# Kernel optimization log

Measured on AMD Instinct MI355X. Metric: run time of the kernel, lower is better.

## Reference

```python
import jax, jax.numpy as jnp
import numpy as np

D_MODEL = 1024
NUM_SLOTS = 64
TOP_K = 8
B, T = 4, 4096


def setup_inputs() -> dict:
    key = jax.random.key(0)
    ks = jax.random.split(key, 16)
    D, S = D_MODEL, NUM_SLOTS
    H = D // 2  # route MLP hidden (hardcoded d_model//2 in source)
    sc = lambda fan_in: 1.0 / np.sqrt(fan_in)
    inp = {
        "x": jax.random.normal(ks[0], (B, T, D), dtype=jnp.float32),
        # learned params
        "slot_init": jax.random.normal(ks[1], (S, D), dtype=jnp.float32) * 0.1,
        "slot_scale": jnp.ones((S, 1), dtype=jnp.float32),
        "w1": jax.random.normal(ks[2], (H, 2 * D), dtype=jnp.float32) * sc(2 * D),
        "b1": jnp.zeros((H,), dtype=jnp.float32),
        "w2": jax.random.normal(ks[3], (S, H), dtype=jnp.float32) * sc(H),
        "b2": jnp.zeros((S,), dtype=jnp.float32),
        "gru_wih": jax.random.normal(ks[4], (3 * D, D), dtype=jnp.float32) * sc(D),
        "gru_whh": jax.random.normal(ks[5], (3 * D, D), dtype=jnp.float32) * sc(D),
        "gru_bih": jnp.zeros((3 * D,), dtype=jnp.float32),
        "gru_bhh": jnp.zeros((3 * D,), dtype=jnp.float32),
        "wv": jax.random.normal(ks[6], (D, D), dtype=jnp.float32) * sc(D),
        "bv": jnp.zeros((D,), dtype=jnp.float32),
        "wo": jax.random.normal(ks[7], (D, D), dtype=jnp.float32) * sc(D),
        "bo": jnp.zeros((D,), dtype=jnp.float32),
        "tau": jnp.ones((1,), dtype=jnp.float32),
    }
    return inp


def _forward(x, slot_init, slot_scale, w1, b1, w2, b2,
             gru_wih, gru_whh, gru_bih, gru_bhh, wv, bv, wo, bo, tau):
    Bn, Tn, D = x.shape
    Sn = slot_init.shape[0]
    # initial slot states, expanded over batch: (B, S, D)
    S = jnp.broadcast_to((slot_init * slot_scale)[None], (Bn, Sn, D)).astype(x.dtype)
    slot_mean = S.mean(axis=1, keepdims=True)                      # (B,1,D)
    ctx = jnp.concatenate([x, jnp.broadcast_to(slot_mean, x.shape)], axis=-1)  # (B,T,2D)
    h = jax.nn.gelu(ctx @ w1.T + b1, approximate=False)
    route_logits = (h @ w2.T + b2) / (jnp.abs(tau) + 0.1)          # (B,T,S)
    topk_vals, topk_idx = jax.lax.top_k(route_logits, TOP_K)
    topk_w = jax.nn.softmax(topk_vals, axis=-1)                    # (B,T,K)
    # scatter top-k weights into dense alpha (B,T,S)
    alpha = jnp.sum(topk_w[..., None] * jax.nn.one_hot(topk_idx, Sn, dtype=x.dtype), axis=-2)
    slot_input = jnp.einsum('bts,btd->bsd', alpha, x)              # dispatch
    slot_wsum = alpha.sum(axis=1) + 1e-8                           # (B,S)
    gi = (slot_input / slot_wsum[..., None]).reshape(Bn * Sn, D)
    hs = S.reshape(Bn * Sn, D)
    # GRUCell (torch semantics)
    gx = gi @ gru_wih.T + gru_bih                                  # (BS, 3D)
    gh = hs @ gru_whh.T + gru_bhh
    xr, xz, xn = jnp.split(gx, 3, axis=-1)
    hr, hz, hn = jnp.split(gh, 3, axis=-1)
    r = jax.nn.sigmoid(xr + hr)
    z = jax.nn.sigmoid(xz + hz)
    n = jnp.tanh(xn + r * hn)
    h_new = (1.0 - z) * n + z * hs
    S_new = h_new.reshape(Bn, Sn, D)
    slot_values = S_new @ wv.T + bv                                # (B,S,D)
    out = jnp.einsum('bts,bsd->btd', alpha, slot_values)           # combine
    return out @ wo.T + bo


def reference(x, slot_init, slot_scale, w1, b1, w2, b2,
              gru_wih, gru_whh, gru_bih, gru_bhh, wv, bv, wo, bo, tau):
    return _forward(x, slot_init, slot_scale, w1, b1, w2, b2,
                    gru_wih, gru_whh, gru_bih, gru_bhh, wv, bv, wo, bo, tau)
```

## Files before the change

### kernel.cpp

```cpp
#include <hip/hip_runtime.h>

using u16 = unsigned short;
using u32 = unsigned int;

typedef __attribute__((ext_vector_type(8))) short bf16x8;
typedef __attribute__((ext_vector_type(4))) float f32x4;

#define NTOK 16384

constexpr size_t OFF_FLAG   = 0;
constexpr size_t OFF_FCNT   = 256;
constexpr size_t OFF_M      = 512;
constexpr size_t OFF_B1P64  = 8704;
constexpr size_t OFF_B1P32  = 12800;
constexpr size_t OFF_B2F    = 14848;
constexpr size_t OFF_BIHF   = 15104;
constexpr size_t OFF_BHHF   = 27392;
constexpr size_t OFF_BVF    = 39680;
constexpr size_t OFF_BOF    = 43776;
constexpr size_t OFF_FLAGS  = 47872;
constexpr size_t OFF_HSHI   = 113408;
constexpr size_t OFF_HSLO   = 244480;
constexpr size_t OFF_HSF    = 375552;
constexpr size_t OFF_GH     = 637696;
constexpr size_t OFF_GIHI   = 1424128;
constexpr size_t OFF_GILO   = 1948416;
constexpr size_t OFF_GX     = 2472704;
constexpr size_t OFF_SNHI   = 5618432;
constexpr size_t OFF_SNLO   = 6142720;
constexpr size_t OFF_SVHI   = 6667008;
constexpr size_t OFF_SVLO   = 7191296;
constexpr size_t OFF_SVO    = 7715584;
constexpr size_t OFF_IDX    = 8764160;
constexpr size_t OFF_WGT    = 9288448;
constexpr size_t OFF_LOGITS = 9812736;
constexpr size_t OFF_W1HI   = 14007040;
constexpr size_t OFF_W1LO   = 16104192;
constexpr size_t OFF_W2HI   = 18201344;
constexpr size_t OFF_W2LO   = 18266880;
constexpr size_t OFF_WIHHI  = 18332416;
constexpr size_t OFF_WIHLO  = 24623872;
constexpr size_t OFF_WHHHI  = 30915328;
constexpr size_t OFF_WHHLO  = 37206784;
constexpr size_t OFF_WVHI   = 43498240;
constexpr size_t OFF_WVLO   = 45595392;
constexpr size_t OFF_WOHI   = 47692544;
constexpr size_t OFF_WOLO   = 49789696;
constexpr size_t OFF_HHI    = 51886848;
constexpr size_t OFF_HLO    = 68664064;
constexpr size_t OFF_DPART  = 85441280;
constexpr size_t OFF_DWSUM  = 93829888;
constexpr size_t OFF_HSMG   = 93838080;
constexpr size_t WS_NEED    = 94886656;

constexpr int QCAP = 256;

__device__ __forceinline__ float bf2f(u16 u) {
  union { u32 i; float f; } c; c.i = ((u32)u) << 16; return c.f;
}
__device__ __forceinline__ u16 f2bf(float f) {
  u32 x = __float_as_uint(f);
  x += 0x7fffu + ((x >> 16) & 1u);
  return (u16)(x >> 16);
}
__device__ __forceinline__ void splitf(float v, u16& hi, u16& lo) {
  hi = f2bf(v);
  lo = f2bf(v - bf2f(hi));
}
__device__ __forceinline__ float rdval(const void* p, int i, int f32m) {
  return f32m ? ((const float*)p)[i] : bf2f(((const u16*)p)[i]);
}
__device__ __forceinline__ void async16(const u16* g, u16* l) {
  __builtin_amdgcn_global_load_lds((const __attribute__((address_space(1))) void*)g,
                                   (__attribute__((address_space(3))) void*)l, 16, 0, 0);
}

__global__ void k_sniff(const u32* __restrict__ w1w, int* __restrict__ flag) {
  int t = threadIdx.x;
  u32 word = w1w[t * 97];
  int ef = (word >> 7) & 0xFF;
  unsigned long long m = __ballot(ef >= 128);
  if (t == 0) flag[0] = (__popcll(m) >= 8) ? 1 : 0;
}

__global__ __launch_bounds__(256) void k_cvt_all(
    const void* __restrict__ w1, const void* __restrict__ w2,
    const void* __restrict__ wih, const void* __restrict__ whh,
    const void* __restrict__ wv, const void* __restrict__ wo,
    const void* __restrict__ b2, const void* __restrict__ bih,
    const void* __restrict__ bhh, const void* __restrict__ bv,
    const void* __restrict__ bo, char* __restrict__ ws,
    const int* __restrict__ flagp)
{
  const int f = *flagp;
  const long long gid = (long long)blockIdx.x * 256 + threadIdx.x;
  const long long C0 = 1048576, C1 = C0 + 32768, C2 = C1 + 3145728,
                  C3 = C2 + 3145728, C4 = C3 + 1048576, C5 = C4 + 1048576;
  if (gid < C5) {
    const void* src; size_t oh, ol; int i;
    if (gid < C0)      { src = w1;  oh = OFF_W1HI;  ol = OFF_W1LO;  i = (int)gid; }
    else if (gid < C1) { src = w2;  oh = OFF_W2HI;  ol = OFF_W2LO;  i = (int)(gid - C0); }
    else if (gid < C2) { src = wih; oh = OFF_WIHHI; ol = OFF_WIHLO; i = (int)(gid - C1); }
    else if (gid < C3) { src = whh; oh = OFF_WHHHI; ol = OFF_WHHLO; i = (int)(gid - C2); }
    else if (gid < C4) { src = wv;  oh = OFF_WVHI;  ol = OFF_WVLO;  i = (int)(gid - C3); }
    else               { src = wo;  oh = OFF_WOHI;  ol = OFF_WOLO;  i = (int)(gid - C4); }
    float v = rdval(src, i, f);
    u16 hi, lo; splitf(v, hi, lo);
    ((u16*)(ws + oh))[i] = hi;
    ((u16*)(ws + ol))[i] = lo;
    return;
  }
  int r = (int)(gid - C5);
  if (r >= 8256) return;
  const void* src; size_t od; int i;
  if (r < 64)        { src = b2;  od = OFF_B2F;  i = r; }
  else if (r < 3136) { src = bih; od = OFF_BIHF; i = r - 64; }
  else if (r < 6208) { src = bhh; od = OFF_BHHF; i = r - 3136; }
  else if (r < 7232) { src = bv;  od = OFF_BVF;  i = r - 6208; }
  else               { src = bo;  od = OFF_BOF;  i = r - 7232; }
  ((float*)(ws + od))[i] = rdval(src, i, f);
}

template<int MODE>
__global__ __launch_bounds__(512, 2) void gemm_bt(
    const u16* __restrict__ Ahi, const u16* __restrict__ Alo,
    const u16* __restrict__ Bhi, const u16* __restrict__ Blo,
    int M, int N, int K, int ldb,
    const float* __restrict__ biasF, float* __restrict__ outF,
    u16* __restrict__ outHi, u16* __restrict__ outLo)
{
  __shared__ alignas(16) u16 smem[2 * 2 * 8192];
  const int t    = threadIdx.x;
  const int grp  = t >> 8;
  const int tl   = t & 255;
  const int wvid = tl >> 6;
  const int lane = t & 63;
  const int quad = lane >> 4;
  const int l16  = lane & 15;
  const int row0 = blockIdx.x * 128;
  const int col0 = blockIdx.y * 128;
  const int wr   = (wvid >> 1) * 64;
  const int wc   = (wvid & 1) * 64;

  const int ra  = tl >> 2;
  const int kqe = (tl & 3) * 8;
  int r_a0 = row0 + ra;      if (r_a0 > M - 1) r_a0 = M - 1;
  int r_a1 = row0 + ra + 64; if (r_a1 > M - 1) r_a1 = M - 1;
  int r_b0 = col0 + ra;      if (r_b0 > N - 1) r_b0 = N - 1;
  int r_b1 = col0 + ra + 64; if (r_b1 > N - 1) r_b1 = N - 1;
  const size_t aoff0 = (size_t)r_a0 * K + kqe;
  const size_t aoff1 = (size_t)r_a1 * K + kqe;
  const size_t boff0 = (size_t)r_b0 * ldb + kqe;
  const size_t boff1 = (size_t)r_b1 * ldb + kqe;

  const int KH  = K >> 1;
  const int NIT = 3 * (KH >> 5);
  int sp = 0, sk = grp * KH;
  const int skend = grp * KH + KH;

  u16* const base = smem + grp * 16384;
  auto stage = [&](int buf) {
    const u16* Ap = (sp == 1) ? Alo : Ahi;
    const u16* Bp = (sp == 2) ? Blo : Bhi;
    u16* At = base + buf * 8192;
    u16* Bt = At + 4096;
    async16(Ap + aoff0 + sk, &At[(wvid * 64) * 8]);
    async16(Ap + aoff1 + sk, &At[(wvid * 64 + 256) * 8]);
    async16(Bp + boff0 + sk, &Bt[(wvid * 64) * 8]);
    async16(Bp + boff1 + sk, &Bt[(wvid * 64 + 256) * 8]);
    sk += 32;
    if (sk == skend) { sk = grp * KH; ++sp; }
  };

  f32x4 acc[4][4] = {};
  stage(0);
  asm volatile("s_waitcnt vmcnt(0)" ::: "memory");
  __syncthreads();
  int cur = 0;
  for (int it = 0; it < NIT; ++it) {
    if (it + 1 < NIT) stage(cur ^ 1);
    const u16* At = base + cur * 8192;
    const u16* Bt = At + 4096;
    bf16x8 af[4], bfr[4];
    #pragma unroll
    for (int mt = 0; mt < 4; ++mt)
      af[mt] = *(const bf16x8*)&At[(wr + mt * 16 + l16) * 32 + quad * 8];
    #pragma unroll
    for (int nt = 0; nt < 4; ++nt)
      bfr[nt] = *(const bf16x8*)&Bt[(wc + nt * 16 + l16) * 32 + quad * 8];
    #pragma unroll
    for (int mt = 0; mt < 4; ++mt)
      #pragma unroll
      for (int nt = 0; nt < 4; ++nt)
        acc[mt][nt] = __builtin_amdgcn_mfma_f32_16x16x32_bf16(
            af[mt], bfr[nt], acc[mt][nt], 0, 0, 0);
    asm volatile("s_waitcnt vmcnt(0)" ::: "memory");
    __syncthreads();
    cur ^= 1;
  }

  float* red = (float*)smem;
  #pragma unroll 1
  for (int half = 0; half < 2; ++half) {
    if (grp == 1 && (wvid & 1) == half) {
      #pragma unroll
      for (int mt = 0; mt < 4; ++mt)
        #pragma unroll
        for (int nt = 0; nt < 4; ++nt)
          #pragma unroll
          for (int r2 = 0; r2 < 4; ++r2)
            red[(wr + mt * 16 + quad * 4 + r2) * 64 + nt * 16 + l16] =
                acc[mt][nt][r2];
    }
    __syncthreads();
    if (grp == 0 && (wvid & 1) == half) {
      #pragma unroll
      for (int mt = 0; mt < 4; ++mt)
        #pragma unroll
        for (int nt = 0; nt < 4; ++nt)
          #pragma unroll
          for (int r2 = 0; r2 < 4; ++r2)
            acc[mt][nt][r2] +=
                red[(wr + mt * 16 + quad * 4 + r2) * 64 + nt * 16 + l16];
    }
    __syncthreads();
  }
  if (grp != 0) return;

  #pragma unroll
  for (int mt = 0; mt < 4; ++mt) {
    #pragma unroll
    for (int nt = 0; nt < 4; ++nt) {
      const int col = col0 + wc + nt * 16 + l16;
      if (col >= N) continue;
      #pragma unroll
      for (int r2 = 0; r2 < 4; ++r2) {
        const int row = row0 + wr + mt * 16 + quad * 4 + r2;
        if (row >= M) continue;
        float v = acc[mt][nt][r2] + biasF[col];
        size_t idx = (size_t)row * N + col;
        if constexpr (MODE == 0) {
          outF[idx] = v;
        } else {
          u16 hi, lo; splitf(v, hi, lo);
          outHi[idx] = hi; outLo[idx] = lo;
        }
      }
    }
  }
}

__global__ __launch_bounds__(256, 4) void gemm_router(
    const void* __restrict__ X,
    const u16* __restrict__ Bhi, const u16* __restrict__ Blo,
    int M, int N, int K, int ldb, const float* __restrict__ biasF,
    u16* __restrict__ outHi, u16* __restrict__ outLo,
    const int* __restrict__ flagp)
{
  __shared__ alignas(16) u16 Athi[64 * 32];
  __shared__ alignas(16) u16 Atlo[64 * 32];
  __shared__ alignas(16) u16 Bthi[128 * 32];
  __shared__ alignas(16) u16 Btlo[128 * 32];
  const int f32m = *flagp;
  const int t    = threadIdx.x;
  const int wvid = t >> 6;
  const int lane = t & 63;
  const int quad = lane >> 4;
  const int l16  = lane & 15;
  const int row0 = blockIdx.x * 64;
  const int col0 = blockIdx.y * 128;
  const int wr   = (wvid >> 1) * 32;
  const int wc   = (wvid & 1) * 64;

  const int ra  = t >> 2;
  const int kqe = (t & 3) * 8;
  int r_b0 = col0 + ra;      if (r_b0 > N - 1) r_b0 = N - 1;
  int r_b1 = col0 + ra + 64; if (r_b1 > N - 1) r_b1 = N - 1;
  const u16* gBhi0 = Bhi + (size_t)r_b0 * ldb + kqe;
  const u16* gBhi1 = Bhi + (size_t)r_b1 * ldb + kqe;
  const u16* gBlo0 = Blo + (size_t)r_b0 * ldb + kqe;
  const u16* gBlo1 = Blo + (size_t)r_b1 * ldb + kqe;

  const float* xsf[2];
  const u16*   xsb[2];
  u16 *adh[2], *adl[2];
  #pragma unroll
  for (int i = 0; i < 2; ++i) {
    int j = t + 256 * i;
    int row = j >> 3, kq = (j & 7) * 4;
    int grow = row0 + row; if (grow > M - 1) grow = M - 1;
    xsf[i] = (const float*)X + (size_t)grow * K + kq;
    xsb[i] = (const u16*)X + (size_t)grow * K + kq;
    adh[i] = &Athi[row * 32 + kq];
    adl[i] = &Atlo[row * 32 + kq];
  }

  f32x4 acc[2][4] = {};
  float4  xv0, xv1;
  ushort4 xb0, xb1;
  if (f32m) { xv0 = *(const float4*)xsf[0];  xv1 = *(const float4*)xsf[1]; }
  else      { xb0 = *(const ushort4*)xsb[0]; xb1 = *(const ushort4*)xsb[1]; }

  for (int k0 = 0; k0 < K; k0 += 32) {
    async16(gBhi0 + k0, &Bthi[(wvid * 64) * 8]);
    async16(gBhi1 + k0, &Bthi[(wvid * 64 + 256) * 8]);
    async16(gBlo0 + k0, &Btlo[(wvid * 64) * 8]);
    async16(gBlo1 + k0, &Btlo[(wvid * 64 + 256) * 8]);
    {
      ushort4 hi4, lo4;
      if (f32m) {
        splitf(xv0.x, hi4.x, lo4.x);
        splitf(xv0.y, hi4.y, lo4.y);
        splitf(xv0.z, hi4.z, lo4.z);
        splitf(xv0.w, hi4.w, lo4.w);
      } else {
        hi4 = xb0; lo4.x = lo4.y = lo4.z = lo4.w = 0;
      }
      *(ushort4*)adh[0] = hi4;
      *(ushort4*)adl[0] = lo4;
      if (f32m) {
        splitf(xv1.x, hi4.x, lo4.x);
        splitf(xv1.y, hi4.y, lo4.y);
        splitf(xv1.z, hi4.z, lo4.z);
        splitf(xv1.w, hi4.w, lo4.w);
      } else {
        hi4 = xb1; lo4.x = lo4.y = lo4.z = lo4.w = 0;
      }
      *(ushort4*)adh[1] = hi4;
      *(ushort4*)adl[1] = lo4;
    }
    if (k0 + 32 < K) {
      if (f32m) {
        xv0 = *(const float4*)(xsf[0] + k0 + 32);
        xv1 = *(const float4*)(xsf[1] + k0 + 32);
      } else {
        xb0 = *(const ushort4*)(xsb[0] + k0 + 32);
        xb1 = *(const ushort4*)(xsb[1] + k0 + 32);
      }
    }
    asm volatile("s_waitcnt vmcnt(0)" ::: "memory");
    __syncthreads();
    bf16x8 ah[2], al[2], bh[4], bl[4];
    #pragma unroll
    for (int mt = 0; mt < 2; ++mt) {
      ah[mt] = *(const bf16x8*)&Athi[(wr + mt * 16 + l16) * 32 + quad * 8];
      al[mt] = *(const bf16x8*)&Atlo[(wr + mt * 16 + l16) * 32 + quad * 8];
    }
    #pragma unroll
    for (int nt = 0; nt < 4; ++nt) {
      bh[nt] = *(const bf16x8*)&Bthi[(wc + nt * 16 + l16) * 32 + quad * 8];
      bl[nt] = *(const bf16x8*)&Btlo[(wc + nt * 16 + l16) * 32 + quad * 8];
    }
    #pragma unroll
    for (int mt = 0; mt < 2; ++mt)
      #pragma unroll
      for (int nt = 0; nt < 4; ++nt) {
        acc[mt][nt] = __builtin_amdgcn_mfma_f32_16x16x32_bf16(
            ah[mt], bh[nt], acc[mt][nt], 0, 0, 0);
        acc[mt][nt] = __builtin_amdgcn_mfma_f32_16x16x32_bf16(
            al[mt], bh[nt], acc[mt][nt], 0, 0, 0);
        acc[mt][nt] = __builtin_amdgcn_mfma_f32_16x16x32_bf16(
            ah[mt], bl[nt], acc[mt][nt], 0, 0, 0);
      }
    __syncthreads();
  }

  #pragma unroll
  for (int mt = 0; mt < 2; ++mt) {
    #pragma unroll
    for (int nt = 0; nt < 4; ++nt) {
      const int col = col0 + wc + nt * 16 + l16;
      if (col >= N) continue;
      #pragma unroll
      for (int r2 = 0; r2 < 4; ++r2) {
        const int row = row0 + wr + mt * 16 + quad * 4 + r2;
        if (row >= M) continue;
        float v = acc[mt][nt][r2] + biasF[col];
        v = 0.5f * v * (1.0f + erff(v * 0.70710678118654752f));
        u16 hi, lo; splitf(v, hi, lo);
        size_t idx = (size_t)row * N + col;
        outHi[idx] = hi; outLo[idx] = lo;
      }
    }
  }
}

__global__ __launch_bounds__(256) void k_init(const void* __restrict__ sli,
    const void* __restrict__ slsc, const int* __restrict__ flagp,
    double* __restrict__ m64, int* __restrict__ fcnt,
    u16* __restrict__ hshi, u16* __restrict__ hslo, float* __restrict__ hsf)
{
  int f = *flagp;
  int gid = blockIdx.x * 256 + threadIdx.x;
  if (gid == 0) fcnt[0] = 0;
  if (gid < 1024) {
    double s = 0.0;
    for (int j = 0; j < 64; ++j)
      s += (double)rdval(sli, j * 1024 + gid, f) * (double)rdval(slsc, j, f);
    m64[gid] = s * (1.0 / 64.0);
  }
  for (int i = gid; i < 64 * 1024; i += 16384) {
    int s = i >> 10;
    float v = rdval(sli, i, f) * rdval(slsc, s, f);
    splitf(v, hshi[i], hslo[i]);
    hsf[i] = v;
  }
}

__global__ __launch_bounds__(256) void k_b1p(const void* __restrict__ w1,
    const void* __restrict__ b1, const int* __restrict__ flagp,
    const double* __restrict__ m64, double* __restrict__ b1p64,
    float* __restrict__ b1p32)
{
  int f = *flagp;
  int h = blockIdx.x * 256 + threadIdx.x;
  if (h >= 512) return;
  double a = (double)rdval(b1, h, f);
  if (f) {
    const float* wr = (const float*)w1 + (size_t)h * 2048 + 1024;
    for (int d = 0; d < 1024; ++d) a += (double)wr[d] * m64[d];
  } else {
    const u16* wr = (const u16*)w1 + (size_t)h * 2048 + 1024;
    for (int d = 0; d < 1024; ++d) a += (double)bf2f(wr[d]) * m64[d];
  }
  b1p64[h] = a;
  b1p32[h] = (float)a;
}

__global__ __launch_bounds__(256) void k_topk(const float* __restrict__ logits,
    const void* __restrict__ tau, const int* __restrict__ flagp,
    int* __restrict__ idxb, float* __restrict__ wgtb,
    int* __restrict__ fcnt, int* __restrict__ flags)
{
  const int f32m = *flagp;
  const int n    = blockIdx.x * 4 + (threadIdx.x >> 6);
  const int lane = threadIdx.x & 63;
  float cur = logits[(size_t)n * 64 + lane];
  float tv[8]; int ti[8]; float v9 = 0.f;
  #pragma unroll
  for (int it = 0; it < 9; ++it) {
    float v = cur; int i = lane;
    #pragma unroll
    for (int off = 32; off; off >>= 1) {
      float ov = __shfl_xor(v, off);
      int   oi = __shfl_xor(i, off);
      if (ov > v || (ov == v && oi < i)) { v = ov; i = oi; }
    }
    if (it < 8) { tv[it] = v; ti[it] = i; if (lane == i) cur = -__builtin_inff(); }
    else v9 = v;
  }
  float itau = 1.0f / (fabsf(rdval(tau, 0, f32m)) + 0.1f);
  float e[8], z = 0.f;
  #pragma unroll
  for (int k = 0; k < 8; ++k) { e[k] = expf((tv[k] - tv[0]) * itau); z += e[k]; }
  if (lane == 0) {
    float theta = f32m ? 2e-4f : 1e-4f;
    if (tv[7] - v9 < theta) { int p = atomicAdd(fcnt, 1); flags[p] = n; }
    float rz = 1.0f / z;
    #pragma unroll
    for (int k = 0; k < 8; ++k) {
      idxb[n * 8 + k] = ti[k];
      wgtb[n * 8 + k] = e[k] * rz;
    }
  }
}

__global__ __launch_bounds__(256) void k_repair_h(const void* __restrict__ x,
    const void* __restrict__ w1, const int* __restrict__ flagp,
    const double* __restrict__ b1p64, const int* __restrict__ fcnt,
    const int* __restrict__ flags, double* __restrict__ hsmg)
{
  const int f = *flagp;
  int cnt = *fcnt; if (cnt > QCAP) cnt = QCAP;
  const int q = blockIdx.x >> 3;
  if (q >= cnt) return;
  const int chunk = blockIdx.x & 7;
  const int n  = flags[q];
  const int wv = threadIdx.x >> 6;
  const int lane = threadIdx.x & 63;

  float xr[16];
  if (f) {
    const float* xp = (const float*)x + (size_t)n * 1024;
    #pragma unroll
    for (int j = 0; j < 16; ++j) xr[j] = xp[lane + 64 * j];
  } else {
    const u16* xp = (const u16*)x + (size_t)n * 1024;
    #pragma unroll
    for (int j = 0; j < 16; ++j) xr[j] = bf2f(xp[lane + 64 * j]);
  }

  const int h0 = chunk * 64 + wv * 16;
  for (int r = 0; r < 16; ++r) {
    const int h = h0 + r;
    double a0 = 0.0, a1 = 0.0;
    if (f) {
      const float* wr = (const float*)w1 + (size_t)h * 2048;
      #pragma unroll
      for (int j = 0; j < 16; j += 2) {
        a0 += (double)xr[j]     * (double)wr[lane + 64 * j];
        a1 += (double)xr[j + 1] * (double)wr[lane + 64 * (j + 1)];
      }
    } else {
      const u16* wr = (const u16*)w1 + (size_t)h * 2048;
      #pragma unroll
      for (int j = 0; j < 16; j += 2) {
        a0 += (double)xr[j]     * (double)bf2f(wr[lane + 64 * j]);
        a1 += (double)xr[j + 1] * (double)bf2f(wr[lane + 64 * (j + 1)]);
      }
    }
    double a = a0 + a1;
    #pragma unroll
    for (int off = 32; off; off >>= 1) a += __shfl_xor(a, off);
    if (lane == 0) {
      a += b1p64[h];
      hsmg[(size_t)q * 512 + h] =
          0.5 * a * (1.0 + erf(a * 0.70710678118654752440));
    }
  }
}

__global__ __launch_bounds__(256) void k_repair_t(const void* __restrict__ x,
    const void* __restrict__ w1, const void* __restrict__ w2,
    const void* __restrict__ b2, const void* __restrict__ tau,
    const int* __restrict__ flagp, const double* __restrict__ b1p64,
    const int* __restrict__ fcnt, const int* __restrict__ flags,
    const double* __restrict__ hsmg, int* __restrict__ idxb,
    float* __restrict__ wgtb)
{
  __shared__ double hsm[512];
  __shared__ double lg[64];
  const int f = *flagp;
  const int cnt = *fcnt;
  const int t = threadIdx.x;
  const int wv = t >> 6;
  const int lane = t & 63;
  for (int q = blockIdx.x; q < cnt; q += gridDim.x) {
    const int n = flags[q];
    if (q < QCAP) {
      for (int h = t; h < 512; h += 256) hsm[h] = hsmg[(size_t)q * 512 + h];
    } else {
      for (int h = wv; h < 512; h += 4) {
        double a0 = 0.0, a1 = 0.0;
        if (f) {
          const float* xp = (const float*)x + (size_t)n * 1024;
          const float* wr = (const float*)w1 + (size_t)h * 2048;
          for (int j = 0; j < 16; j += 2) {
            a0 += (double)xp[lane + 64 * j]       * (double)wr[lane + 64 * j];
            a1 += (double)xp[lane + 64 * (j + 1)] * (double)wr[lane + 64 * (j + 1)];
          }
        } else {
          const u16* xp = (const u16*)x + (size_t)n * 1024;
          const u16* wr = (const u16*)w1 + (size_t)h * 2048;
          for (int j = 0; j < 16; j += 2) {
            a0 += (double)bf2f(xp[lane + 64 * j]) * (double)bf2f(wr[lane + 64 * j]);
            a1 += (double)bf2f(xp[lane + 64 * (j + 1)]) *
                  (double)bf2f(wr[lane + 64 * (j + 1)]);
          }
        }
        double a = a0 + a1;
        #pragma unroll
        for (int off = 32; off; off >>= 1) a += __shfl_xor(a, off);
        if (lane == 0) {
          a += b1p64[h];
          hsm[h] = 0.5 * a * (1.0 + erf(a * 0.70710678118654752440));
        }
      }
    }
    __syncthreads();
    for (int s = wv; s < 64; s += 4) {
      double a0 = 0.0, a1 = 0.0;
      if (f) {
        const float* wr = (const float*)w2 + (size_t)s * 512;
        #pragma unroll
        for (int j = 0; j < 8; j += 2) {
          a0 += hsm[lane + 64 * j]       * (double)wr[lane + 64 * j];
          a1 += hsm[lane + 64 * (j + 1)] * (double)wr[lane + 64 * (j + 1)];
        }
      } else {
        const u16* wr = (const u16*)w2 + (size_t)s * 512;
        #pragma unroll
        for (int j = 0; j < 8; j += 2) {
          a0 += hsm[lane + 64 * j]       * (double)bf2f(wr[lane + 64 * j]);
          a1 += hsm[lane + 64 * (j + 1)] * (double)bf2f(wr[lane + 64 * (j + 1)]);
        }
      }
      double a = a0 + a1;
      #pragma unroll
      for (int off = 32; off; off >>= 1) a += __shfl_xor(a, off);
      if (lane == 0) lg[s] = a + (double)rdval(b2, s, f);
    }
    __syncthreads();
    if (t == 0) {
      double tv = fabs((double)rdval(tau, 0, f)) + 0.1;
      double vals[8]; int ids[8];
      for (int it = 0; it < 8; ++it) {
        double best = -1e300; int bi = 0;
        for (int i = 0; i < 64; ++i)
          if (lg[i] > best) { best = lg[i]; bi = i; }
        vals[it] = best; ids[it] = bi; lg[bi] = -1e300;
      }
      double e[8], z = 0.0;
      for (int k = 0; k < 8; ++k) { e[k] = exp((vals[k] - vals[0]) / tv); z += e[k]; }
      for (int k = 0; k < 8; ++k) {
        idxb[n * 8 + k] = ids[k];
        wgtb[n * 8 + k] = (float)(e[k] / z);
      }
    }
    __syncthreads();
  }
}

__global__ __launch_bounds__(256) void k_dispatch(const void* __restrict__ X,
    const int* __restrict__ flagp, const int* __restrict__ idxb,
    const float* __restrict__ wgtb,
    float* __restrict__ dpart, float* __restrict__ dwsum)
{
  __shared__ int   ltok[512];
  __shared__ float lw[512];
  __shared__ int   lcnt;
  __shared__ float lws;
  const int f32m = *flagp;
  const int g    = blockIdx.x;
  const int xcd  = g & 7;
  const int ord  = g >> 3;
  const int win  = xcd * 4 + (ord >> 6);
  const int s    = ord & 63;
  const int b     = win >> 3;
  const int chunk = win & 7;
  const int t     = threadIdx.x;
  if (t == 0) { lcnt = 0; lws = 0.f; }
  __syncthreads();
  const int tok0 = b * 4096 + chunk * 512;
  float mysum = 0.f;
  for (int tok = tok0 + t; tok < tok0 + 512; tok += 256) {
    int hit = -1;
    #pragma unroll
    for (int k = 0; k < 8; ++k)
      if (idxb[(size_t)tok * 8 + k] == s) hit = k;
    if (hit >= 0) {
      float w = wgtb[(size_t)tok * 8 + hit];
      int p = atomicAdd(&lcnt, 1);
      ltok[p] = tok; lw[p] = w;
      mysum += w;
    }
  }
  atomicAdd(&lws, mysum);
  __syncthreads();
  const int cnt = lcnt;
  float a0 = 0.f, a1 = 0.f, a2 = 0.f, a3 = 0.f;
  if (f32m) {
    const float* Xf = (const float*)X;
    for (int e = 0; e < cnt; ++e) {
      int tok = ltok[e]; float w = lw[e];
      const float4 v = *(const float4*)(Xf + (size_t)tok * 1024 + 4 * t);
      a0 += w * v.x; a1 += w * v.y; a2 += w * v.z; a3 += w * v.w;
    }
  } else {
    const u16* Xb = (const u16*)X;
    for (int e = 0; e < cnt; ++e) {
      int tok = ltok[e]; float w = lw[e];
      const ushort4 v = *(const ushort4*)(Xb + (size_t)tok * 1024 + 4 * t);
      a0 += w * bf2f(v.x); a1 += w * bf2f(v.y);
      a2 += w * bf2f(v.z); a3 += w * bf2f(v.w);
    }
  }
  const int bs = b * 64 + s;
  float* pp = dpart + ((size_t)bs * 8 + chunk) * 1024 + 4 * t;
  float4 outv = { a0, a1, a2, a3 };
  *(float4*)pp = outv;
  if (t == 0) dwsum[bs * 8 + chunk] = lws;
}

__global__ __launch_bounds__(256) void k_dreduce(const float* __restrict__ dpart,
    const float* __restrict__ dwsum, u16* __restrict__ gihi, u16* __restrict__ gilo)
{
  const int bs = blockIdx.x;
  const int t  = threadIdx.x;
  float ws = 0.f;
  #pragma unroll
  for (int c = 0; c < 8; ++c) ws += dwsum[bs * 8 + c];
  const float inv = 1.0f / (ws + 1e-8f);
  float a0 = 0.f, a1 = 0.f, a2 = 0.f, a3 = 0.f;
  const float* pb = dpart + (size_t)bs * 8 * 1024 + 4 * t;
  #pragma unroll
  for (int c = 0; c < 8; ++c) {
    const float4 v = *(const float4*)(pb + c * 1024);
    a0 += v.x; a1 += v.y; a2 += v.z; a3 += v.w;
  }
  const size_t base = (size_t)bs * 1024 + 4 * t;
  splitf(a0 * inv, gihi[base + 0], gilo[base + 0]);
  splitf(a1 * inv, gihi[base + 1], gilo[base + 1]);
  splitf(a2 * inv, gihi[base + 2], gilo[base + 2]);
  splitf(a3 * inv, gihi[base + 3], gilo[base + 3]);
}

__global__ __launch_bounds__(256) void k_gru(const float* __restrict__ gx,
    const float* __restrict__ gh, const float* __restrict__ hsf,
    u16* __restrict__ snhi, u16* __restrict__ snlo)
{
  int gid = blockIdx.x * 256 + threadIdx.x;
  int r = gid >> 10, d = gid & 1023, s = r & 63;
  const float* gxr = gx + (size_t)r * 3072;
  const float* ghr = gh + (size_t)s * 3072;
  float rr = 1.0f / (1.0f + expf(-(gxr[d] + ghr[d])));
  float zz = 1.0f / (1.0f + expf(-(gxr[1024 + d] + ghr[1024 + d])));
  float nn = tanhf(gxr[2048 + d] + rr * ghr[2048 + d]);
  float hs = hsf[s * 1024 + d];
  float hv = (1.0f - zz) * nn + zz * hs;
  splitf(hv, snhi[gid], snlo[gid]);
}

__global__ __launch_bounds__(256) void k_out(const int* __restrict__ idxb,
    const float* __restrict__ wgtb, const float* __restrict__ svo,
    const int* __restrict__ flagp, void* __restrict__ out)
{
  const int f32m = *flagp;
  int n = blockIdx.x * 4 + (threadIdx.x >> 6);
  int lane = threadIdx.x & 63;
  int b = n >> 12;
  const float* svb = svo + (size_t)b * 64 * 1024;
  int id[8]; float w[8];
  #pragma unroll
  for (int k = 0; k < 8; ++k) { id[k] = idxb[n * 8 + k]; w[k] = wgtb[n * 8 + k]; }
  #pragma unroll
  for (int i = 0; i < 16; ++i) {
    int d = i * 64 + lane;
    float a = 0.f;
    #pragma unroll
    for (int k = 0; k < 8; ++k) a += w[k] * svb[(size_t)id[k] * 1024 + d];
    size_t idx = (size_t)n * 1024 + d;
    if (f32m) ((float*)out)[idx] = a;
    else      ((u16*)out)[idx] = f2bf(a);
  }
}

extern "C" void kernel_launch(void* const* d_in, const int* in_sizes, int n_in,
                              void* d_out, int out_size, void* d_ws, size_t ws_size,
                              hipStream_t stream) {
  if (ws_size < WS_NEED) {
    hipMemsetAsync(d_out, 0, (size_t)out_size * 2, stream);
    return;
  }
  const void* x    = d_in[0];
  const void* sli  = d_in[1];
  const void* slsc = d_in[2];
  const void* w1   = d_in[3];
  const void* b1   = d_in[4];
  const void* w2   = d_in[5];
  const void* b2   = d_in[6];
  const void* wih  = d_in[7];
  const void* whh  = d_in[8];
  const void* bih  = d_in[9];
  const void* bhh  = d_in[10];
  const void* wv   = d_in[11];
  const void* bv   = d_in[12];
  const void* wo   = d_in[13];
  const void* bo   = d_in[14];
  const void* tau  = d_in[15];
  char* ws = (char*)d_ws;

  int*    flag   = (int*)(ws + OFF_FLAG);
  int*    fcnt   = (int*)(ws + OFF_FCNT);
  double* m64    = (double*)(ws + OFF_M);
  double* b1p64  = (double*)(ws + OFF_B1P64);
  float*  b1p32  = (float*)(ws + OFF_B1P32);
  float*  b2f    = (float*)(ws + OFF_B2F);
  float*  bihf   = (float*)(ws + OFF_BIHF);
  float*  bhhf   = (float*)(ws + OFF_BHHF);
  float*  bvf    = (float*)(ws + OFF_BVF);
  float*  bof    = (float*)(ws + OFF_BOF);
  int*    flags  = (int*)(ws + OFF_FLAGS);
  u16*    hshi   = (u16*)(ws + OFF_HSHI);
  u16*    hslo   = (u16*)(ws + OFF_HSLO);
  float*  hsf    = (float*)(ws + OFF_HSF);
  float*  gh     = (float*)(ws + OFF_GH);
  u16*    gihi   = (u16*)(ws + OFF_GIHI);
  u16*    gilo   = (u16*)(ws + OFF_GILO);
  float*  gx     = (float*)(ws + OFF_GX);
  u16*    snhi   = (u16*)(ws + OFF_SNHI);
  u16*    snlo   = (u16*)(ws + OFF_SNLO);
  u16*    svhi   = (u16*)(ws + OFF_SVHI);
  u16*    svlo   = (u16*)(ws + OFF_SVLO);
  float*  svo    = (float*)(ws + OFF_SVO);
  int*    idxb   = (int*)(ws + OFF_IDX);
  float*  wgtb   = (float*)(ws + OFF_WGT);
  float*  logits = (float*)(ws + OFF_LOGITS);
  u16*    w1hi   = (u16*)(ws + OFF_W1HI);
  u16*    w1lo   = (u16*)(ws + OFF_W1LO);
  u16*    w2hi   = (u16*)(ws + OFF_W2HI);
  u16*    w2lo   = (u16*)(ws + OFF_W2LO);
  u16*    wihhi  = (u16*)(ws + OFF_WIHHI);
  u16*    wihlo  = (u16*)(ws + OFF_WIHLO);
  u16*    whhhi  = (u16*)(ws + OFF_WHHHI);
  u16*    whhlo  = (u16*)(ws + OFF_WHHLO);
  u16*    wvhi   = (u16*)(ws + OFF_WVHI);
  u16*    wvlo   = (u16*)(ws + OFF_WVLO);
  u16*    wohi   = (u16*)(ws + OFF_WOHI);
  u16*    wolo   = (u16*)(ws + OFF_WOLO);
  u16*    hhi    = (u16*)(ws + OFF_HHI);
  u16*    hlo    = (u16*)(ws + OFF_HLO);
  float*  dpart  = (float*)(ws + OFF_DPART);
  float*  dwsum  = (float*)(ws + OFF_DWSUM);
  double* hsmg   = (double*)(ws + OFF_HSMG);

  k_sniff<<<1, 64, 0, stream>>>((const u32*)w1, flag);

  k_init<<<64, 256, 0, stream>>>(sli, slsc, flag, m64, fcnt, hshi, hslo, hsf);
  k_b1p<<<2, 256, 0, stream>>>(w1, b1, flag, m64, b1p64, b1p32);

  k_cvt_all<<<37025, 256, 0, stream>>>(w1, w2, wih, whh, wv, wo,
                                       b2, bih, bhh, bv, bo, ws, flag);

  gemm_bt<0><<<dim3(1, 24), 512, 0, stream>>>(
      hshi, hslo, whhhi, whhlo, 64, 3072, 1024, 1024, bhhf, gh, nullptr, nullptr);

  gemm_router<<<dim3(256, 4), 256, 0, stream>>>(
      x, w1hi, w1lo, NTOK, 512, 1024, 2048, b1p32, hhi, hlo, flag);

  gemm_bt<0><<<dim3(128, 1), 512, 0, stream>>>(
      hhi, hlo, w2hi, w2lo, NTOK, 64, 512, 512, b2f, logits, nullptr, nullptr);

  k_topk<<<4096, 256, 0, stream>>>(logits, tau, flag, idxb, wgtb, fcnt, flags);
  k_repair_h<<<2048, 256, 0, stream>>>(x, w1, flag, b1p64, fcnt, flags, hsmg);
  k_repair_t<<<256, 256, 0, stream>>>(x, w1, w2, b2, tau, flag, b1p64, fcnt,
                                      flags, hsmg, idxb, wgtb);
  k_dispatch<<<2048, 256, 0, stream>>>(x, flag, idxb, wgtb, dpart, dwsum);
  k_dreduce<<<256, 256, 0, stream>>>(dpart, dwsum, gihi, gilo);

  gemm_bt<0><<<dim3(2, 24), 512, 0, stream>>>(
      gihi, gilo, wihhi, wihlo, 256, 3072, 1024, 1024, bihf, gx, nullptr, nullptr);

  k_gru<<<1024, 256, 0, stream>>>(gx, gh, hsf, snhi, snlo);

  gemm_bt<3><<<dim3(2, 8), 512, 0, stream>>>(
      snhi, snlo, wvhi, wvlo, 256, 1024, 1024, 1024, bvf, nullptr, svhi, svlo);

  gemm_bt<0><<<dim3(2, 8), 512, 0, stream>>>(
      svhi, svlo, wohi, wolo, 256, 1024, 1024, 1024, bof, svo, nullptr, nullptr);

  k_out<<<4096, 256, 0, stream>>>(idxb, wgtb, svo, flag, d_out);

  (void)in_sizes; (void)n_in; (void)out_size; (void)ws_size;
}
```

Before: 657.2 us.

## Restructure dispatch to stream token chunks once with LDS atomic accumulation

The dispatch kernel previously had each block handle one (batch, slot, 512-token chunk) and gather the X rows routed to that slot, so each X row was read up to eight times. Now each block takes a 256-token chunk, a 256-wide slice of d and half of the slots. It streams X once per (chunk, d-slice, slot-half) and scatters weighted values into a 32x256 LDS accumulator with shared-memory atomics. The partial buffers move into the reused hidden-activation workspace region, and the reduce kernel now sums 16 chunks instead of 8. The trade-off is heavy LDS atomic traffic, one per token-k pair, and a larger partial buffer to write and reduce.

```diff
diff --git a/kernel.cpp b/kernel.cpp
--- a/kernel.cpp
+++ b/kernel.cpp
@@ -48,8 +48,8 @@
 constexpr size_t OFF_WOLO   = 49789696;
 constexpr size_t OFF_HHI    = 51886848;
 constexpr size_t OFF_HLO    = 68664064;
-constexpr size_t OFF_DPART  = 85441280;
-constexpr size_t OFF_DWSUM  = 93829888;
+constexpr size_t OFF_DP2    = 51886848;
+constexpr size_t OFF_DW2    = 68664064;
 constexpr size_t OFF_HSMG   = 93838080;
 constexpr size_t WS_NEED    = 94886656;
 
@@ -616,60 +616,57 @@
     const float* __restrict__ wgtb,
     float* __restrict__ dpart, float* __restrict__ dwsum)
 {
-  __shared__ int   ltok[512];
-  __shared__ float lw[512];
-  __shared__ int   lcnt;
-  __shared__ float lws;
+  __shared__ float sacc[32][256];
+  __shared__ int   lidx[2048];
+  __shared__ float lwgt[2048];
+  __shared__ float swsum[32];
   const int f32m = *flagp;
-  const int g    = blockIdx.x;
-  const int xcd  = g & 7;
-  const int ord  = g >> 3;
-  const int win  = xcd * 4 + (ord >> 6);
-  const int s    = ord & 63;
-  const int b     = win >> 3;
-  const int chunk = win & 7;
-  const int t     = threadIdx.x;
-  if (t == 0) { lcnt = 0; lws = 0.f; }
+  const int g  = blockIdx.x;
+  const int sh = g & 1;
+  const int ch = (g >> 1) & 15;
+  const int dq = (g >> 5) & 3;
+  const int b  = g >> 7;
+  const int t  = threadIdx.x;
+
+  float4* sz = (float4*)sacc;
+  #pragma unroll
+  for (int i = 0; i < 8; ++i) sz[t + 256 * i] = float4{0.f, 0.f, 0.f, 0.f};
+  if (t < 32) swsum[t] = 0.f;
+  const int tok0 = b * 4096 + ch * 256;
+  for (int i = t; i < 2048; i += 256) {
+    lidx[i] = idxb[(size_t)tok0 * 8 + i];
+    lwgt[i] = wgtb[(size_t)tok0 * 8 + i];
+  }
   __syncthreads();
-  const int tok0 = b * 4096 + chunk * 512;
-  float mysum = 0.f;
-  for (int tok = tok0 + t; tok < tok0 + 512; tok += 256) {
-    int hit = -1;
-    #pragma unroll
-    for (int k = 0; k < 8; ++k)
-      if (idxb[(size_t)tok * 8 + k] == s) hit = k;
-    if (hit >= 0) {
-      float w = wgtb[(size_t)tok * 8 + hit];
-      int p = atomicAdd(&lcnt, 1);
-      ltok[p] = tok; lw[p] = w;
-      mysum += w;
-    }
-  }
-  atomicAdd(&lws, mysum);
+
+  const int d = dq * 256 + t;
+  const float* Xf = (const float*)X;
+  const u16*   Xb = (const u16*)X;
+  for (int j = 0; j < 256; ++j) {
+    float xv = f32m ? Xf[(size_t)(tok0 + j) * 1024 + d]
+                    : bf2f(Xb[(size_t)(tok0 + j) * 1024 + d]);
+    #pragma unroll
+    for (int k = 0; k < 8; ++k) {
+      int ik = lidx[j * 8 + k];
+      if ((ik >> 5) == sh) {
+        atomicAdd(&sacc[ik & 31][t], lwgt[j * 8 + k] * xv);
+      }
+    }
+  }
+  if (dq == 0) {
+    for (int i = t; i < 2048; i += 256) {
+      int ik = lidx[i];
+      if ((ik >> 5) == sh) atomicAdd(&swsum[ik & 31], lwgt[i]);
+    }
+  }
   __syncthreads();
-  const int cnt = lcnt;
-  float a0 = 0.f, a1 = 0.f, a2 = 0.f, a3 = 0.f;
-  if (f32m) {
-    const float* Xf = (const float*)X;
-    for (int e = 0; e < cnt; ++e) {
-      int tok = ltok[e]; float w = lw[e];
-      const float4 v = *(const float4*)(Xf + (size_t)tok * 1024 + 4 * t);
-      a0 += w * v.x; a1 += w * v.y; a2 += w * v.z; a3 += w * v.w;
-    }
-  } else {
-    const u16* Xb = (const u16*)X;
-    for (int e = 0; e < cnt; ++e) {
-      int tok = ltok[e]; float w = lw[e];
-      const ushort4 v = *(const ushort4*)(Xb + (size_t)tok * 1024 + 4 * t);
-      a0 += w * bf2f(v.x); a1 += w * bf2f(v.y);
-      a2 += w * bf2f(v.z); a3 += w * bf2f(v.w);
-    }
-  }
-  const int bs = b * 64 + s;
-  float* pp = dpart + ((size_t)bs * 8 + chunk) * 1024 + 4 * t;
-  float4 outv = { a0, a1, a2, a3 };
-  *(float4*)pp = outv;
-  if (t == 0) dwsum[bs * 8 + chunk] = lws;
+
+  const int slo = sh * 32;
+  #pragma unroll 4
+  for (int s = 0; s < 32; ++s)
+    dpart[((size_t)(b * 64 + slo + s) * 16 + ch) * 1024 + d] = sacc[s][t];
+  if (dq == 0 && t < 32)
+    dwsum[(b * 64 + slo + t) * 16 + ch] = swsum[t];
 }
 
 __global__ __launch_bounds__(256) void k_dreduce(const float* __restrict__ dpart,
@@ -679,12 +676,12 @@
   const int t  = threadIdx.x;
   float ws = 0.f;
   #pragma unroll
-  for (int c = 0; c < 8; ++c) ws += dwsum[bs * 8 + c];
+  for (int c = 0; c < 16; ++c) ws += dwsum[bs * 16 + c];
   const float inv = 1.0f / (ws + 1e-8f);
   float a0 = 0.f, a1 = 0.f, a2 = 0.f, a3 = 0.f;
-  const float* pb = dpart + (size_t)bs * 8 * 1024 + 4 * t;
-  #pragma unroll
-  for (int c = 0; c < 8; ++c) {
+  const float* pb = dpart + (size_t)bs * 16 * 1024 + 4 * t;
+  #pragma unroll
+  for (int c = 0; c < 16; ++c) {
     const float4 v = *(const float4*)(pb + c * 1024);
     a0 += v.x; a1 += v.y; a2 += v.z; a3 += v.w;
   }
@@ -800,8 +797,8 @@
   u16*    wolo   = (u16*)(ws + OFF_WOLO);
   u16*    hhi    = (u16*)(ws + OFF_HHI);
   u16*    hlo    = (u16*)(ws + OFF_HLO);
-  float*  dpart  = (float*)(ws + OFF_DPART);
-  float*  dwsum  = (float*)(ws + OFF_DWSUM);
+  float*  dpart  = (float*)(ws + OFF_DP2);
+  float*  dwsum  = (float*)(ws + OFF_DW2);
   double* hsmg   = (double*)(ws + OFF_HSMG);
 
   k_sniff<<<1, 64, 0, stream>>>((const u32*)w1, flag);
@@ -825,7 +822,7 @@
   k_repair_h<<<2048, 256, 0, stream>>>(x, w1, flag, b1p64, fcnt, flags, hsmg);
   k_repair_t<<<256, 256, 0, stream>>>(x, w1, w2, b2, tau, flag, b1p64, fcnt,
                                       flags, hsmg, idxb, wgtb);
-  k_dispatch<<<2048, 256, 0, stream>>>(x, flag, idxb, wgtb, dpart, dwsum);
+  k_dispatch<<<512, 256, 0, stream>>>(x, flag, idxb, wgtb, dpart, dwsum);
   k_dreduce<<<256, 256, 0, stream>>>(dpart, dwsum, gihi, gilo);
 
   gemm_bt<0><<<dim3(2, 24), 512, 0, stream>>>(
```

Result: slower. 1.373 ms (+108.9%).
